# Kernel tuning notes

Measured on AMD Instinct MI355X. Metric: run time of the kernel, lower is better.

The kernel has to match this reference:

```python
import jax, jax.numpy as jnp
import numpy as np

D_MODEL = 1024
NUM_HEADS = 16
HEAD_DIM = D_MODEL // NUM_HEADS
FF_DIM = 4096
EPS = 1e-5


def _layer_norm(x, gamma, beta):
    mu = jnp.mean(x, axis=-1, keepdims=True)
    var = jnp.var(x, axis=-1, keepdims=True)
    return (x - mu) * jax.lax.rsqrt(var + EPS) * gamma + beta


def setup_inputs() -> dict:
    key0 = jax.random.key(0)
    ks = jax.random.split(key0, 20)
    s = 0.02
    B, S = 2, 2048
    inp = {
        'value': jax.random.normal(ks[0], (B, S, D_MODEL), jnp.float32),
        'key': jax.random.normal(ks[1], (B, S, D_MODEL), jnp.float32),
        'query': jax.random.normal(ks[2], (B, S, D_MODEL), jnp.float32),
        # attention projections (stored [in, out]; y = x @ W + b)
        'wq': jax.random.normal(ks[3], (D_MODEL, D_MODEL), jnp.float32) * s,
        'bq': jnp.zeros((D_MODEL,), jnp.float32),
        'wk': jax.random.normal(ks[4], (D_MODEL, D_MODEL), jnp.float32) * s,
        'bk': jnp.zeros((D_MODEL,), jnp.float32),
        'wv': jax.random.normal(ks[5], (D_MODEL, D_MODEL), jnp.float32) * s,
        'bv': jnp.zeros((D_MODEL,), jnp.float32),
        'wo': jax.random.normal(ks[6], (D_MODEL, D_MODEL), jnp.float32) * s,
        'bo': jnp.zeros((D_MODEL,), jnp.float32),
        # layernorm 1
        'g1': jnp.ones((D_MODEL,), jnp.float32),
        'beta1': jnp.zeros((D_MODEL,), jnp.float32),
        # feed-forward
        'w1': jax.random.normal(ks[7], (D_MODEL, FF_DIM), jnp.float32) * s,
        'b1': jnp.zeros((FF_DIM,), jnp.float32),
        'w2': jax.random.normal(ks[8], (FF_DIM, D_MODEL), jnp.float32) * s,
        'b2': jnp.zeros((D_MODEL,), jnp.float32),
        # layernorm 2
        'g2': jnp.ones((D_MODEL,), jnp.float32),
        'beta2': jnp.zeros((D_MODEL,), jnp.float32),
    }
    return inp


def reference(value, key, query, wq, bq, wk, bk, wv, bv, wo, bo,
              g1, beta1, w1, b1, w2, b2, g2, beta2):
    B, S, _ = query.shape
    # QKV projections -> [B, S, H, Dh]
    Q = (query @ wq + bq).reshape(B, S, NUM_HEADS, HEAD_DIM)
    K = (key @ wk + bk).reshape(B, S, NUM_HEADS, HEAD_DIM)
    V = (value @ wv + bv).reshape(B, S, NUM_HEADS, HEAD_DIM)
    # scaled dot-product attention (full score matrix, as in source)
    energy = jnp.einsum('bqhd,bkhd->bhqk', Q, K) / jnp.sqrt(jnp.float32(HEAD_DIM))
    attn = jax.nn.softmax(energy, axis=-1)
    out = jnp.einsum('bhqk,bkhd->bqhd', attn, V).reshape(B, S, D_MODEL)
    attn_out = out @ wo + bo
    # residual + norm1 (dropout is identity in eval)
    x = _layer_norm(attn_out + query, g1, beta1)
    # feed-forward
    ff = jax.nn.relu(x @ w1 + b1) @ w2 + b2
    # residual + norm2
    return _layer_norm(ff + x, g2, beta2)
```

## Files before the change

kernel.cpp:

```cpp
#include <hip/hip_runtime.h>
#include <hip/hip_bf16.h>
#include <cstdint>
#include <math.h>

typedef __bf16 bf16_t;
typedef __attribute__((ext_vector_type(2))) __bf16 bf16x2;
typedef __attribute__((ext_vector_type(4))) __bf16 bf16x4;
typedef __attribute__((ext_vector_type(8))) __bf16 bf16x8;
typedef __attribute__((ext_vector_type(4))) float f32x4;
typedef __attribute__((ext_vector_type(16))) float f32x16;
typedef __attribute__((ext_vector_type(2))) int int2v;
typedef __attribute__((ext_vector_type(4))) int int4v;

#define B_SZ 2
#define S_SZ 2048
#define D_MODEL 1024
#define NUM_HEADS 16
#define HEAD_DIM 64
#define FF_DIM 4096
#define M_ROWS (B_SZ * S_SZ)

#define CF 0.180336880f
#define THRC 2.0f

__device__ __forceinline__ float fexp2(float x) { return __builtin_amdgcn_exp2f(x); }

__device__ __forceinline__ void gload_lds16(const void* g, void* lds) {
    __builtin_amdgcn_global_load_lds(
        (const __attribute__((address_space(1))) void*)(uintptr_t)g,
        (__attribute__((address_space(3))) void*)(uint32_t)(uintptr_t)lds,
        16, 0, 0);
}

__device__ __forceinline__ f32x4 mfma16(bf16x8 a, bf16x8 b, f32x4 c) {
    return __builtin_amdgcn_mfma_f32_16x16x32_bf16(a, b, c, 0, 0, 0);
}
__device__ __forceinline__ f32x16 mfma32(bf16x8 a, bf16x8 b, f32x16 c) {
    return __builtin_amdgcn_mfma_f32_32x32x16_bf16(a, b, c, 0, 0, 0);
}
__device__ __forceinline__ int2v plswap(int a, int b) {
    return __builtin_amdgcn_permlane32_swap(a, b, false, false);
}
__device__ __forceinline__ int packbf(float a, float b) {
    bf16x2 t; t[0] = (bf16_t)a; t[1] = (bf16_t)b;
    return __builtin_bit_cast(int, t);
}

__device__ __forceinline__ int xcd_swz(int lin, int nwg) {
    return (lin & 7) * (nwg >> 3) + (lin >> 3);
}

__global__ __launch_bounds__(256) void prep_all(
    const float* __restrict__ q, const float* __restrict__ k, const float* __restrict__ v,
    bf16_t* __restrict__ qb, bf16_t* __restrict__ kb, bf16_t* __restrict__ vb,
    const float* __restrict__ wq, const float* __restrict__ wk,
    const float* __restrict__ wv, const float* __restrict__ wo,
    const float* __restrict__ w1, const float* __restrict__ w2,
    bf16_t* __restrict__ wqT, bf16_t* __restrict__ wkT,
    bf16_t* __restrict__ wvT, bf16_t* __restrict__ woT,
    bf16_t* __restrict__ w1T, bf16_t* __restrict__ w2T) {
    __shared__ float t[32][33];
    const int id = blockIdx.x;
    const int tid = threadIdx.x;
    if (id >= 12288) {
        const int t2 = id - 12288;
        const int which = t2 >> 12, blk = t2 & 4095;
        const float* in = which == 0 ? q : which == 1 ? k : v;
        bf16_t* out = which == 0 ? qb : which == 1 ? kb : vb;
        size_t i = ((size_t)blk * 256 + tid) * 4;
        float4 vv = *(const float4*)(in + i);
        bf16x4 o;
        o[0] = (bf16_t)vv.x; o[1] = (bf16_t)vv.y; o[2] = (bf16_t)vv.z; o[3] = (bf16_t)vv.w;
        *(bf16x4*)(out + i) = o;
        return;
    }
    const float* W; bf16_t* WT; int K, N, k0, n0;
    if (id < 4096) {
        const int z = id >> 10, t3 = id & 1023;
        W = z == 0 ? wq : z == 1 ? wk : z == 2 ? wv : wo;
        WT = z == 0 ? wqT : z == 1 ? wkT : z == 2 ? wvT : woT;
        K = 1024; N = 1024; k0 = (t3 & 31) * 32; n0 = (t3 >> 5) * 32;
    } else if (id < 8192) {
        const int t3 = id - 4096;
        W = w1; WT = w1T; K = 1024; N = 4096;
        k0 = (t3 & 31) * 32; n0 = (t3 >> 5) * 32;
    } else {
        const int t3 = id - 8192;
        W = w2; WT = w2T; K = 4096; N = 1024;
        k0 = (t3 & 127) * 32; n0 = (t3 >> 7) * 32;
    }
    const int rr = tid >> 3, cc = (tid & 7) * 4;
    float4 vv = *(const float4*)(W + (size_t)(k0 + rr) * N + n0 + cc);
    t[rr][cc + 0] = vv.x; t[rr][cc + 1] = vv.y; t[rr][cc + 2] = vv.z; t[rr][cc + 3] = vv.w;
    __syncthreads();
    bf16x4 o;
    o[0] = (bf16_t)t[cc + 0][rr]; o[1] = (bf16_t)t[cc + 1][rr];
    o[2] = (bf16_t)t[cc + 2][rr]; o[3] = (bf16_t)t[cc + 3][rr];
    *(bf16x4*)(WT + (size_t)(n0 + rr) * K + k0 + cc) = o;
}

template<int NJT, bool RELU, bool OUT_BF16, bool OUT_F32>
__device__ __forceinline__ void gemm8p_core(const bf16_t* __restrict__ Ag, int lda,
                                            const bf16_t* __restrict__ Bg, int ldb,
                                            const float* __restrict__ bias, bool useBias,
                                            float* __restrict__ Cf,
                                            bf16_t* __restrict__ Cb,
                                            int N, int Klen, int m0, int n0,
                                            bf16_t* sA, bf16_t* sB,
                                            bf16_t* __restrict__ VTt) {
    constexpr int BELE = 8192 * NJT;
    constexpr int NBQ = 2 * NJT;
    const int tid = threadIdx.x;
    const int lane = tid & 63, w = tid >> 6;
    const int l31 = lane & 31, hi = lane >> 5;
    const int wm = (w >> 2) * 128;
    const int wn = (w & 3) * (32 * NJT);
    const int rs7 = l31 & 7;

    const int scol = ((tid & 7) ^ ((tid >> 3) & 7)) * 8;
    const bf16_t* aSrc = Ag + (size_t)(m0 + (tid >> 3)) * lda + scol;
    const bf16_t* bSrc = Bg + (size_t)(n0 + (tid >> 3)) * ldb + scol;

    f32x16 acc[4][NJT];
#pragma unroll
    for (int it = 0; it < 4; it++)
#pragma unroll
        for (int jt = 0; jt < NJT; jt++)
#pragma unroll
            for (int e = 0; e < 16; e++) acc[it][jt][e] = 0.f;

    auto stA = [&](int buf, int q, int k0) {
        gload_lds16(aSrc + (size_t)(q * 64) * lda + k0, sA + buf * 16384 + q * 4096 + tid * 8);
    };
    auto stB = [&](int buf, int q, int k0) {
        gload_lds16(bSrc + (size_t)(q * 64) * ldb + k0, sB + buf * BELE + q * 4096 + tid * 8);
    };

    bf16x8 a[4], b[NJT];
    auto RD = [&](int buf, int ks) {
        const bf16_t* bA = sA + buf * 16384;
        const bf16_t* bB = sB + buf * BELE;
        const int cs = ((((ks << 1) | hi)) ^ rs7) << 3;
#pragma unroll
        for (int it = 0; it < 4; it++)
            a[it] = *(const bf16x8*)(bA + (wm + it * 32 + l31) * 64 + cs);
#pragma unroll
        for (int jt = 0; jt < NJT; jt++)
            b[jt] = *(const bf16x8*)(bB + (wn + jt * 32 + l31) * 64 + cs);
    };
    auto MM = [&]() {
        __builtin_amdgcn_s_setprio(1);
#pragma unroll
        for (int it = 0; it < 4; it++)
#pragma unroll
            for (int jt = 0; jt < NJT; jt++)
                acc[it][jt] = mfma32(a[it], b[jt], acc[it][jt]);
        __builtin_amdgcn_s_setprio(0);
    };

#define LGKM0() do { asm volatile("s_waitcnt lgkmcnt(0)" ::: "memory"); \
                     __builtin_amdgcn_sched_barrier(0); } while (0)

    const int nk = Klen >> 6;
#pragma unroll
    for (int q = 0; q < 4; q++) stA(0, q, 0);
#pragma unroll
    for (int q = 0; q < NBQ; q++) stB(0, q, 0);
    asm volatile("s_waitcnt vmcnt(0)" ::: "memory");
    __builtin_amdgcn_s_barrier();

    for (int t = 0; t < nk; ++t) {
        const int buf = t & 1, nb = buf ^ 1;
        const int kn = (t + 1) << 6;
        const bool hn = (t + 1 < nk);
        RD(buf, 0);
        if (hn) { stA(nb, 0, kn); stA(nb, 1, kn); stA(nb, 2, kn); }
        LGKM0();
        MM();
        RD(buf, 1);
        if (hn) { stA(nb, 3, kn); stB(nb, 0, kn); if (NBQ > 1) stB(nb, 1, kn); }
        LGKM0();
        MM();
        RD(buf, 2);
        if (hn && NBQ > 2) { stB(nb, 2, kn); stB(nb, 3, kn); }
        LGKM0();
        MM();
        RD(buf, 3);
        LGKM0();
        MM();
        asm volatile("s_waitcnt vmcnt(0)" ::: "memory");
        __builtin_amdgcn_s_barrier();
    }
#undef LGKM0

    if (VTt) {
#pragma unroll
        for (int it = 0; it < 4; it++) {
#pragma unroll
            for (int jt = 0; jt < NJT; jt++) {
                const int n = n0 + wn + jt * 32 + l31;
                const float bv = bias[n];
                const int hh = n >> 6, dd = n & 63;
#pragma unroll
                for (int rq = 0; rq < 4; rq++) {
                    bf16x4 st;
#pragma unroll
                    for (int i2 = 0; i2 < 4; i2++)
                        st[i2] = (bf16_t)(acc[it][jt][rq * 4 + i2] + bv);
                    const int mrow = m0 + wm + it * 32 + rq * 8 + hi * 4;
                    const int bb = mrow >> 11, s = mrow & 2047;
                    *(bf16x4*)(VTt + (((size_t)(bb * 16 + hh)) * 64 + dd) * 2048 + s) = st;
                }
            }
        }
        return;
    }
#pragma unroll
    for (int it = 0; it < 4; it++) {
#pragma unroll
        for (int jt = 0; jt < NJT; jt++) {
            const int n = n0 + wn + jt * 32 + l31;
            const float bv = useBias ? bias[n] : 0.f;
#pragma unroll
            for (int e = 0; e < 16; e++) {
                const int mrow = m0 + wm + it * 32 + (e & 3) + ((e >> 2) << 3) + hi * 4;
                float val = acc[it][jt][e] + bv;
                if (RELU) val = fmaxf(val, 0.f);
                if (OUT_F32) Cf[(size_t)mrow * N + n] = val;
                if (OUT_BF16) Cb[(size_t)mrow * N + n] = (bf16_t)val;
            }
        }
    }
}

template<int NJT, bool RELU>
__global__ __launch_bounds__(512, 1) void gemm8p(const bf16_t* __restrict__ A, int lda,
                                                 const bf16_t* __restrict__ Bt, int ldb,
                                                 const float* __restrict__ bias,
                                                 bf16_t* __restrict__ Cb0,
                                                 bf16_t* __restrict__ Cb1,
                                                 int N, int Klen) {
    __shared__ bf16_t sA[2 * 16384];
    __shared__ bf16_t sB[2 * 8192 * NJT];
    const int lin = blockIdx.x + gridDim.x * (blockIdx.y + gridDim.y * blockIdx.z);
    const int nwg = gridDim.x * gridDim.y * gridDim.z;
    const int sz = xcd_swz(lin, nwg);
    const int bx = sz % gridDim.x;
    const int rest = sz / gridDim.x;
    const int by = rest % gridDim.y;
    const int bz = rest / gridDim.y;
    const int koff = bz * Klen;
    gemm8p_core<NJT, RELU, true, false>(A + koff, lda, Bt + koff, ldb,
                                        bias, bz == 0,
                                        nullptr, bz ? Cb1 : Cb0, N, Klen,
                                        bx * 256, by * (128 * NJT), sA, sB, nullptr);
}

template<int NJT, bool RELU>
__global__ __launch_bounds__(512, 1) void gemm8p_b(const bf16_t* __restrict__ A, int lda,
                                                   const bf16_t* __restrict__ Bt, int ldb,
                                                   const float* __restrict__ bias,
                                                   bf16_t* __restrict__ Cb,
                                                   int N, int Klen) {
    __shared__ bf16_t sA[2 * 16384];
    __shared__ bf16_t sB[2 * 8192 * NJT];
    const int lin = blockIdx.x + gridDim.x * (blockIdx.y + gridDim.y * blockIdx.z);
    const int nwg = gridDim.x * gridDim.y * gridDim.z;
    const int sz = xcd_swz(lin, nwg);
    const int bx = sz % gridDim.x;
    const int rest = sz / gridDim.x;
    const int by = rest % gridDim.y;
    gemm8p_core<NJT, RELU, true, false>(A, lda, Bt, ldb, bias, true,
                                        nullptr, Cb, N, Klen,
                                        bx * 256, by * (128 * NJT), sA, sB, nullptr);
}

__global__ __launch_bounds__(512, 1) void gemm_qkv8p(const bf16_t* __restrict__ A0,
                                                     const bf16_t* __restrict__ A1,
                                                     const bf16_t* __restrict__ A2,
                                                     const bf16_t* __restrict__ B0,
                                                     const bf16_t* __restrict__ B1,
                                                     const bf16_t* __restrict__ B2,
                                                     const float* __restrict__ b0,
                                                     const float* __restrict__ b1,
                                                     const float* __restrict__ b2,
                                                     bf16_t* __restrict__ C0,
                                                     bf16_t* __restrict__ C1,
                                                     bf16_t* __restrict__ VTout) {
    __shared__ bf16_t sA[2 * 16384];
    __shared__ bf16_t sB[2 * 16384];
    const int lin = blockIdx.x + gridDim.x * (blockIdx.y + gridDim.y * blockIdx.z);
    const int nwg = gridDim.x * gridDim.y * gridDim.z;
    const int sz = xcd_swz(lin, nwg);
    const int bx = sz % gridDim.x;
    const int rest = sz / gridDim.x;
    const int by = rest % gridDim.y;
    const int bz = rest / gridDim.y;
    const bf16_t* A = bz == 0 ? A0 : bz == 1 ? A1 : A2;
    const bf16_t* Bt = bz == 0 ? B0 : bz == 1 ? B1 : B2;
    const float* bias = bz == 0 ? b0 : bz == 1 ? b1 : b2;
    bf16_t* C = bz == 0 ? C0 : bz == 1 ? C1 : nullptr;
    bf16_t* VTt = bz == 2 ? VTout : nullptr;
    gemm8p_core<2, false, true, false>(A, 1024, Bt, 1024, bias, true,
                                       nullptr, C, 1024, 1024, bx * 256, by * 256,
                                       sA, sB, VTt);
}

__device__ __forceinline__ void flash_tile(
    const char* kt, const char* vt, int l31, int hi,
    const bf16x8 (&bq)[4],
    f32x16& o0, f32x16& o1, float& mC, float& l_run)
{
    bf16x8 ak[4];
#pragma unroll
    for (int kb = 0; kb < 4; kb++)
        ak[kb] = *(const bf16x8*)(kt + l31 * 128 + (((kb << 1) | hi) ^ (l31 & 7)) * 16);
    bf16x8 av[4];
#pragma unroll
    for (int db = 0; db < 2; db++)
#pragma unroll
        for (int kb = 0; kb < 2; kb++)
            av[db * 2 + kb] = *(const bf16x8*)(vt + (db * 32 + l31) * 64 + ((((kb << 1) | hi)) ^ ((l31 >> 1) & 3)) * 16);

    f32x16 s;
#pragma unroll
    for (int e = 0; e < 16; e++) s[e] = 0.f;
#pragma unroll
    for (int kb = 0; kb < 4; kb++) s = mfma32(ak[kb], bq[kb], s);

    float ma = fmaxf(fmaxf(s[0], s[1]), fmaxf(s[2], s[3]));
    float mb = fmaxf(fmaxf(s[4], s[5]), fmaxf(s[6], s[7]));
    float mc = fmaxf(fmaxf(s[8], s[9]), fmaxf(s[10], s[11]));
    float md = fmaxf(fmaxf(s[12], s[13]), fmaxf(s[14], s[15]));
    float pmaxC = fmaxf(fmaxf(ma, mb), fmaxf(mc, md)) * CF;

    if (!__all(pmaxC <= mC + THRC)) {
        int2v pr = plswap(__float_as_int(pmaxC), __float_as_int(pmaxC));
        float rowmaxC = fmaxf(__int_as_float(pr[0]), __int_as_float(pr[1]));
        float mnewC = fmaxf(mC, rowmaxC);
        float alpha = fexp2(mC - mnewC);
        mC = mnewC;
        l_run *= alpha;
#pragma unroll
        for (int e = 0; e < 16; e++) { o0[e] *= alpha; o1[e] *= alpha; }
    }

#pragma unroll
    for (int e = 0; e < 16; e++) s[e] = fexp2(__builtin_fmaf(s[e], CF, -mC));
    float t0 = (s[0] + s[1]) + (s[2] + s[3]);
    float t1 = (s[4] + s[5]) + (s[6] + s[7]);
    float t2 = (s[8] + s[9]) + (s[10] + s[11]);
    float t3 = (s[12] + s[13]) + (s[14] + s[15]);
    l_run += (t0 + t1) + (t2 + t3);

#pragma unroll
    for (int kb2 = 0; kb2 < 2; kb2++) {
        const int bse = kb2 * 8;
        int W0 = packbf(s[bse + 0], s[bse + 1]);
        int W1 = packbf(s[bse + 2], s[bse + 3]);
        int W2 = packbf(s[bse + 4], s[bse + 5]);
        int W3 = packbf(s[bse + 6], s[bse + 7]);
        int2v r02 = plswap(W0, W2);
        int2v r13 = plswap(W1, W3);
        int4v fw; fw[0] = r02[0]; fw[1] = r13[0]; fw[2] = r02[1]; fw[3] = r13[1];
        bf16x8 pf = __builtin_bit_cast(bf16x8, fw);
        o0 = mfma32(av[kb2], pf, o0);
        o1 = mfma32(av[2 + kb2], pf, o1);
    }
}

__global__ __launch_bounds__(256) void flash_attn(const bf16_t* __restrict__ Qp,
                                                  const bf16_t* __restrict__ Kp,
                                                  const bf16_t* __restrict__ VT,
                                                  bf16_t* __restrict__ Oa) {
    __shared__ alignas(16) char lds[2][2][8192];
    const int tid = threadIdx.x;
    const int lane = tid & 63;
    const int wave = tid >> 6;
    const int half = wave >> 1;
    const int qt = wave & 1;
    const int l31 = lane & 31, hi = lane >> 5;

    const int lin = blockIdx.x + (blockIdx.y << 5) + (blockIdx.z << 9);
    const int swz = (lin & 7) * 128 + (lin >> 3);
    const int qb = swz & 31;
    const int h = (swz >> 5) & 15;
    const int b = swz >> 9;

    const int q0 = qb * 64 + qt * 32;

    const bf16_t* Qb = Qp + (size_t)b * S_SZ * D_MODEL + h * HEAD_DIM;
    const bf16_t* Kb = Kp + (size_t)b * S_SZ * D_MODEL + h * HEAD_DIM;
    const bf16_t* Vb = VT + ((size_t)(b * NUM_HEADS + h) * HEAD_DIM) * S_SZ;

    const int sh = wave & 1;
    const int skvbase = sh * (S_SZ / 2);
    const bool kRole = wave < 2;

    const bf16_t* src_run;
    size_t inner_stride;
    size_t tile_stride;
    char* dst0;
    char* dst1;
    if (kRole) {
        src_run = Kb + (size_t)(skvbase + (lane >> 3)) * D_MODEL + ((lane & 7) ^ (lane >> 3)) * 8;
        inner_stride = (size_t)8 * D_MODEL;
        tile_stride = (size_t)32 * D_MODEL;
        dst0 = &lds[0][sh][0] + lane * 16;
        dst1 = &lds[1][sh][0] + lane * 16;
    } else {
        src_run = Vb + (size_t)(lane >> 2) * S_SZ + skvbase + ((lane & 3) ^ ((lane >> 3) & 3)) * 8;
        inner_stride = (size_t)16 * S_SZ;
        tile_stride = 32;
        dst0 = &lds[0][sh][4096] + lane * 16;
        dst1 = &lds[1][sh][4096] + lane * 16;
    }

    bf16x8 bq[4];
#pragma unroll
    for (int kb = 0; kb < 4; kb++)
        bq[kb] = *(const bf16x8*)(Qb + (size_t)(q0 + l31) * D_MODEL + kb * 16 + hi * 8);

    f32x16 o0, o1;
#pragma unroll
    for (int e = 0; e < 16; e++) { o0[e] = 0.f; o1[e] = 0.f; }
    float mC = -1e30f, l_run = 0.f;

    const char* kt0 = &lds[0][half][0];
    const char* vt0 = &lds[0][half][4096];
    const char* kt1 = &lds[1][half][0];
    const char* vt1 = &lds[1][half][4096];

#pragma unroll
    for (int ii = 0; ii < 4; ii++)
        gload_lds16(src_run + ii * inner_stride, dst0 + ii * 1024);
    src_run += tile_stride;
    __syncthreads();

    for (int t = 0; t < 32; t += 2) {
#pragma unroll
        for (int ii = 0; ii < 4; ii++)
            gload_lds16(src_run + ii * inner_stride, dst1 + ii * 1024);
        src_run += tile_stride;
        flash_tile(kt0, vt0, l31, hi, bq, o0, o1, mC, l_run);
        __syncthreads();

        if (t + 2 < 32) {
#pragma unroll
            for (int ii = 0; ii < 4; ii++)
                gload_lds16(src_run + ii * inner_stride, dst0 + ii * 1024);
            src_run += tile_stride;
        }
        flash_tile(kt1, vt1, l31, hi, bq, o0, o1, mC, l_run);
        __syncthreads();
    }

    int2v lp = plswap(__float_as_int(l_run), __float_as_int(l_run));
    l_run = __int_as_float(lp[0]) + __int_as_float(lp[1]);

    float (*obuf)[2][64] = (float (*)[2][64])(&lds[0][0][0]);
    float (*mrg)[64][2] = (float (*)[64][2])(&lds[0][0][0] + 16384);
    if (half == 1) {
        mrg[qt][lane][0] = mC;
        mrg[qt][lane][1] = l_run;
#pragma unroll
        for (int e = 0; e < 16; e++) {
            obuf[e][qt][lane] = o0[e];
            obuf[16 + e][qt][lane] = o1[e];
        }
    }
    __syncthreads();
    if (half == 0) {
        const float m2C = mrg[qt][lane][0], l2 = mrg[qt][lane][1];
        const float mm = fmaxf(mC, m2C);
        const float e1 = fexp2(mC - mm);
        const float e2 = fexp2(m2C - mm);
        const float linv = 1.f / (l_run * e1 + l2 * e2);
        bf16_t* Orow = Oa + ((size_t)b * S_SZ + q0 + l31) * D_MODEL + h * HEAD_DIM;
#pragma unroll
        for (int db = 0; db < 2; db++) {
#pragma unroll
            for (int rq = 0; rq < 4; rq++) {
                bf16x4 st;
#pragma unroll
                for (int i = 0; i < 4; i++) {
                    const int e = rq * 4 + i;
                    const float own = db ? o1[e] : o0[e];
                    const float oth = obuf[db * 16 + e][qt][lane];
                    st[i] = (bf16_t)((own * e1 + oth * e2) * linv);
                }
                *(bf16x4*)(Orow + db * 32 + rq * 8 + hi * 4) = st;
            }
        }
    }
}

__global__ __launch_bounds__(256) void ln_fused(const bf16_t* __restrict__ A,
                                                const bf16_t* __restrict__ A2,
                                                const bf16_t* __restrict__ R,
                                                const float* __restrict__ gamma,
                                                const float* __restrict__ beta,
                                                float* __restrict__ Xf,
                                                bf16_t* __restrict__ Xb) {
    __shared__ float red[8];
    int row = blockIdx.x, tid = threadIdx.x;
    size_t base = (size_t)row * D_MODEL + tid * 4;
    bf16x4 a = *(const bf16x4*)(A + base);
    bf16x4 a2 = *(const bf16x4*)(A2 + base);
    bf16x4 rv = *(const bf16x4*)(R + base);
    float v0 = (float)a[0] + (float)a2[0] + (float)rv[0];
    float v1 = (float)a[1] + (float)a2[1] + (float)rv[1];
    float v2 = (float)a[2] + (float)a2[2] + (float)rv[2];
    float v3 = (float)a[3] + (float)a2[3] + (float)rv[3];
    float s = v0 + v1 + v2 + v3;
    float q = v0 * v0 + v1 * v1 + v2 * v2 + v3 * v3;
#pragma unroll
    for (int off = 32; off; off >>= 1) { s += __shfl_down(s, off); q += __shfl_down(q, off); }
    if ((tid & 63) == 0) { red[tid >> 6] = s; red[4 + (tid >> 6)] = q; }
    __syncthreads();
    s = red[0] + red[1] + red[2] + red[3];
    q = red[4] + red[5] + red[6] + red[7];
    float mean = s * (1.f / D_MODEL);
    float var = q * (1.f / D_MODEL) - mean * mean;
    float rstd = rsqrtf(var + 1e-5f);
    float4 gm = *(const float4*)(gamma + tid * 4);
    float4 bt = *(const float4*)(beta + tid * 4);
    float y0 = (v0 - mean) * rstd * gm.x + bt.x;
    float y1 = (v1 - mean) * rstd * gm.y + bt.y;
    float y2 = (v2 - mean) * rstd * gm.z + bt.z;
    float y3 = (v3 - mean) * rstd * gm.w + bt.w;
    if (Xf) {
        float4 yo; yo.x = y0; yo.y = y1; yo.z = y2; yo.w = y3;
        *(float4*)(Xf + base) = yo;
    }
    if (Xb) {
        bf16x4 ob; ob[0] = (bf16_t)y0; ob[1] = (bf16_t)y1; ob[2] = (bf16_t)y2; ob[3] = (bf16_t)y3;
        *(bf16x4*)(Xb + base) = ob;
    }
}

extern "C" void kernel_launch(void* const* d_in, const int* in_sizes, int n_in,
                              void* d_out, int out_size, void* d_ws, size_t ws_size,
                              hipStream_t stream) {
    const float* value = (const float*)d_in[0];
    const float* key   = (const float*)d_in[1];
    const float* query = (const float*)d_in[2];
    const float* wq = (const float*)d_in[3];
    const float* bq = (const float*)d_in[4];
    const float* wk = (const float*)d_in[5];
    const float* bk = (const float*)d_in[6];
    const float* wv = (const float*)d_in[7];
    const float* bv = (const float*)d_in[8];
    const float* wo = (const float*)d_in[9];
    const float* bo = (const float*)d_in[10];
    const float* g1 = (const float*)d_in[11];
    const float* beta1 = (const float*)d_in[12];
    const float* w1 = (const float*)d_in[13];
    const float* b1 = (const float*)d_in[14];
    const float* w2 = (const float*)d_in[15];
    const float* b2 = (const float*)d_in[16];
    const float* g2 = (const float*)d_in[17];
    const float* beta2 = (const float*)d_in[18];
    (void)in_sizes; (void)n_in; (void)out_size; (void)ws_size;

    const size_t MB = 1ull << 20;
    char* ws = (char*)d_ws;
    bf16_t* wqT = (bf16_t*)(ws + 0 * MB);
    bf16_t* wkT = (bf16_t*)(ws + 2 * MB);
    bf16_t* wvT = (bf16_t*)(ws + 4 * MB);
    bf16_t* woT = (bf16_t*)(ws + 6 * MB);
    bf16_t* w1T = (bf16_t*)(ws + 8 * MB);
    bf16_t* w2T = (bf16_t*)(ws + 16 * MB);
    bf16_t* q_bf = (bf16_t*)(ws + 24 * MB);
    bf16_t* k_bf = (bf16_t*)(ws + 32 * MB);
    bf16_t* v_bf = (bf16_t*)(ws + 40 * MB);
    bf16_t* Qp  = (bf16_t*)(ws + 48 * MB);
    bf16_t* Kp  = (bf16_t*)(ws + 56 * MB);
    bf16_t* VT  = (bf16_t*)(ws + 64 * MB);
    bf16_t* attn = (bf16_t*)(ws + 88 * MB);
    bf16_t* woP0 = (bf16_t*)(ws + 32 * MB);
    bf16_t* woP1 = (bf16_t*)(ws + 42 * MB);
    bf16_t* x_b = (bf16_t*)(ws + 96 * MB);
    bf16_t* h_b = (bf16_t*)(ws + 32 * MB);
    bf16_t* ffP0 = (bf16_t*)(ws + 64 * MB);
    bf16_t* ffP1 = (bf16_t*)(ws + 72 * MB);

    dim3 blk(256);
    dim3 blk512(512);

    prep_all<<<24576, blk, 0, stream>>>(query, key, value, q_bf, k_bf, v_bf,
                                        wq, wk, wv, wo, w1, w2,
                                        wqT, wkT, wvT, woT, w1T, w2T);

    gemm_qkv8p<<<dim3(16, 4, 3), blk512, 0, stream>>>(q_bf, k_bf, v_bf, wqT, wkT, wvT,
                                                      bq, bk, bv, Qp, Kp, VT);

    flash_attn<<<dim3(32, 16, 2), blk, 0, stream>>>(Qp, Kp, VT, attn);

    gemm8p<1, false><<<dim3(16, 8, 2), blk512, 0, stream>>>(attn, 1024, woT, 1024, bo, woP0, woP1, D_MODEL, 512);

    ln_fused<<<4096, blk, 0, stream>>>(woP0, woP1, q_bf, g1, beta1, nullptr, x_b);

    gemm8p_b<2, true><<<dim3(16, 16, 1), blk512, 0, stream>>>(x_b, 1024, w1T, 1024, b1, h_b, FF_DIM, 1024);

    gemm8p<1, false><<<dim3(16, 8, 2), blk512, 0, stream>>>(h_b, 4096, w2T, 4096, b2, ffP0, ffP1, D_MODEL, 2048);

    ln_fused<<<4096, blk, 0, stream>>>(ffP0, ffP1, x_b, g2, beta2, (float*)d_out, nullptr);
}
```

Baseline: 221.7 us.

## Restructure flash attention to single-wave blocks with full KV sweep per wave

Changes flash attention from 4-wave blocks, where the KV sequence was split across wave pairs and merged through LDS, to single-wave blocks that each process 32 queries over the whole KV range. Each wave loads both its K and V tiles itself, and double buffering now relies on vmcnt waits instead of __syncthreads, which removes the LDS merge and block barriers. The cost is that each K/V tile is now fetched by one wave for only 32 queries instead of 64, roughly doubling KV global/L2 traffic, and each wave runs twice as many serial tiles.

```diff
diff --git a/kernel.cpp b/kernel.cpp
--- a/kernel.cpp
+++ b/kernel.cpp
@@ -369,52 +369,46 @@
     }
 }
 
-__global__ __launch_bounds__(256) void flash_attn(const bf16_t* __restrict__ Qp,
-                                                  const bf16_t* __restrict__ Kp,
-                                                  const bf16_t* __restrict__ VT,
-                                                  bf16_t* __restrict__ Oa) {
-    __shared__ alignas(16) char lds[2][2][8192];
-    const int tid = threadIdx.x;
-    const int lane = tid & 63;
-    const int wave = tid >> 6;
-    const int half = wave >> 1;
-    const int qt = wave & 1;
+__global__ __launch_bounds__(64) void flash_attn(const bf16_t* __restrict__ Qp,
+                                                 const bf16_t* __restrict__ Kp,
+                                                 const bf16_t* __restrict__ VT,
+                                                 bf16_t* __restrict__ Oa) {
+    __shared__ alignas(16) char lds[2][8192];
+    const int lane = threadIdx.x;
     const int l31 = lane & 31, hi = lane >> 5;
 
-    const int lin = blockIdx.x + (blockIdx.y << 5) + (blockIdx.z << 9);
-    const int swz = (lin & 7) * 128 + (lin >> 3);
-    const int qb = swz & 31;
-    const int h = (swz >> 5) & 15;
-    const int b = swz >> 9;
-
-    const int q0 = qb * 64 + qt * 32;
+    const int lin = blockIdx.x + (blockIdx.y << 6) + (blockIdx.z << 10);
+    const int swz = (lin & 7) * 256 + (lin >> 3);
+    const int qb = swz & 63;
+    const int h = (swz >> 6) & 15;
+    const int b = swz >> 10;
+
+    const int q0 = qb * 32;
 
     const bf16_t* Qb = Qp + (size_t)b * S_SZ * D_MODEL + h * HEAD_DIM;
     const bf16_t* Kb = Kp + (size_t)b * S_SZ * D_MODEL + h * HEAD_DIM;
     const bf16_t* Vb = VT + ((size_t)(b * NUM_HEADS + h) * HEAD_DIM) * S_SZ;
 
-    const int sh = wave & 1;
-    const int skvbase = sh * (S_SZ / 2);
-    const bool kRole = wave < 2;
-
-    const bf16_t* src_run;
-    size_t inner_stride;
-    size_t tile_stride;
-    char* dst0;
-    char* dst1;
-    if (kRole) {
-        src_run = Kb + (size_t)(skvbase + (lane >> 3)) * D_MODEL + ((lane & 7) ^ (lane >> 3)) * 8;
-        inner_stride = (size_t)8 * D_MODEL;
-        tile_stride = (size_t)32 * D_MODEL;
-        dst0 = &lds[0][sh][0] + lane * 16;
-        dst1 = &lds[1][sh][0] + lane * 16;
-    } else {
-        src_run = Vb + (size_t)(lane >> 2) * S_SZ + skvbase + ((lane & 3) ^ ((lane >> 3) & 3)) * 8;
-        inner_stride = (size_t)16 * S_SZ;
-        tile_stride = 32;
-        dst0 = &lds[0][sh][4096] + lane * 16;
-        dst1 = &lds[1][sh][4096] + lane * 16;
-    }
+    const bf16_t* srcK = Kb + (size_t)(lane >> 3) * D_MODEL + ((lane & 7) ^ (lane >> 3)) * 8;
+    const bf16_t* srcV = Vb + (size_t)(lane >> 2) * S_SZ + ((lane & 3) ^ ((lane >> 3) & 3)) * 8;
+
+    char* dK0 = &lds[0][0] + lane * 16;
+    char* dK1 = &lds[1][0] + lane * 16;
+    char* dV0 = &lds[0][4096] + lane * 16;
+    char* dV1 = &lds[1][4096] + lane * 16;
+
+#define STG(BUF, T) do { \
+    const bf16_t* sk_ = srcK + (size_t)((T) * 32) * D_MODEL; \
+    const bf16_t* sv_ = srcV + (T) * 32; \
+    char* dk_ = (BUF) ? dK1 : dK0; \
+    char* dv_ = (BUF) ? dV1 : dV0; \
+    _Pragma("unroll") \
+    for (int ii = 0; ii < 4; ii++) \
+        gload_lds16(sk_ + (size_t)(ii * 8) * D_MODEL, dk_ + ii * 1024); \
+    _Pragma("unroll") \
+    for (int ii = 0; ii < 4; ii++) \
+        gload_lds16(sv_ + (size_t)(ii * 16) * S_SZ, dv_ + ii * 1024); \
+} while (0)
 
     bf16x8 bq[4];
 #pragma unroll
@@ -426,71 +420,37 @@
     for (int e = 0; e < 16; e++) { o0[e] = 0.f; o1[e] = 0.f; }
     float mC = -1e30f, l_run = 0.f;
 
-    const char* kt0 = &lds[0][half][0];
-    const char* vt0 = &lds[0][half][4096];
-    const char* kt1 = &lds[1][half][0];
-    const char* vt1 = &lds[1][half][4096];
-
-#pragma unroll
-    for (int ii = 0; ii < 4; ii++)
-        gload_lds16(src_run + ii * inner_stride, dst0 + ii * 1024);
-    src_run += tile_stride;
-    __syncthreads();
-
-    for (int t = 0; t < 32; t += 2) {
-#pragma unroll
-        for (int ii = 0; ii < 4; ii++)
-            gload_lds16(src_run + ii * inner_stride, dst1 + ii * 1024);
-        src_run += tile_stride;
-        flash_tile(kt0, vt0, l31, hi, bq, o0, o1, mC, l_run);
-        __syncthreads();
-
-        if (t + 2 < 32) {
-#pragma unroll
-            for (int ii = 0; ii < 4; ii++)
-                gload_lds16(src_run + ii * inner_stride, dst0 + ii * 1024);
-            src_run += tile_stride;
+    STG(0, 0);
+    for (int t = 0; t < 64; ++t) {
+        const int buf = t & 1;
+        if (t + 1 < 64) {
+            STG(buf ^ 1, t + 1);
+            asm volatile("s_waitcnt vmcnt(8)" ::: "memory");
+        } else {
+            asm volatile("s_waitcnt vmcnt(0)" ::: "memory");
         }
-        flash_tile(kt1, vt1, l31, hi, bq, o0, o1, mC, l_run);
-        __syncthreads();
-    }
+        __builtin_amdgcn_sched_barrier(0);
+        flash_tile(buf ? &lds[1][0] : &lds[0][0],
+                   buf ? &lds[1][4096] : &lds[0][4096],
+                   l31, hi, bq, o0, o1, mC, l_run);
+    }
+#undef STG
 
     int2v lp = plswap(__float_as_int(l_run), __float_as_int(l_run));
     l_run = __int_as_float(lp[0]) + __int_as_float(lp[1]);
-
-    float (*obuf)[2][64] = (float (*)[2][64])(&lds[0][0][0]);
-    float (*mrg)[64][2] = (float (*)[64][2])(&lds[0][0][0] + 16384);
-    if (half == 1) {
-        mrg[qt][lane][0] = mC;
-        mrg[qt][lane][1] = l_run;
-#pragma unroll
-        for (int e = 0; e < 16; e++) {
-            obuf[e][qt][lane] = o0[e];
-            obuf[16 + e][qt][lane] = o1[e];
-        }
-    }
-    __syncthreads();
-    if (half == 0) {
-        const float m2C = mrg[qt][lane][0], l2 = mrg[qt][lane][1];
-        const float mm = fmaxf(mC, m2C);
-        const float e1 = fexp2(mC - mm);
-        const float e2 = fexp2(m2C - mm);
-        const float linv = 1.f / (l_run * e1 + l2 * e2);
-        bf16_t* Orow = Oa + ((size_t)b * S_SZ + q0 + l31) * D_MODEL + h * HEAD_DIM;
-#pragma unroll
-        for (int db = 0; db < 2; db++) {
-#pragma unroll
-            for (int rq = 0; rq < 4; rq++) {
-                bf16x4 st;
-#pragma unroll
-                for (int i = 0; i < 4; i++) {
-                    const int e = rq * 4 + i;
-                    const float own = db ? o1[e] : o0[e];
-                    const float oth = obuf[db * 16 + e][qt][lane];
-                    st[i] = (bf16_t)((own * e1 + oth * e2) * linv);
-                }
-                *(bf16x4*)(Orow + db * 32 + rq * 8 + hi * 4) = st;
+    const float linv = 1.f / l_run;
+    bf16_t* Orow = Oa + ((size_t)b * S_SZ + q0 + l31) * D_MODEL + h * HEAD_DIM;
+#pragma unroll
+    for (int db = 0; db < 2; db++) {
+#pragma unroll
+        for (int rq = 0; rq < 4; rq++) {
+            bf16x4 st;
+#pragma unroll
+            for (int i = 0; i < 4; i++) {
+                const int e = rq * 4 + i;
+                st[i] = (bf16_t)((db ? o1[e] : o0[e]) * linv);
             }
+            *(bf16x4*)(Orow + db * 32 + rq * 8 + hi * 4) = st;
         }
     }
 }
@@ -595,7 +555,7 @@
     gemm_qkv8p<<<dim3(16, 4, 3), blk512, 0, stream>>>(q_bf, k_bf, v_bf, wqT, wkT, wvT,
                                                       bq, bk, bv, Qp, Kp, VT);
 
-    flash_attn<<<dim3(32, 16, 2), blk, 0, stream>>>(Qp, Kp, VT, attn);
+    flash_attn<<<dim3(64, 16, 2), dim3(64), 0, stream>>>(Qp, Kp, VT, attn);
 
     gemm8p<1, false><<<dim3(16, 8, 2), blk512, 0, stream>>>(attn, 1024, woT, 1024, bo, woP0, woP1, D_MODEL, 512);
 
```

New measurement: 248.5 us. +12.1%, slower.
